# Optimization experiments

Measured on AMD Instinct MI355X. Metric: run time of the kernel, lower is better.

The kernel has to match this reference:

```python
import jax, jax.numpy as jnp
import numpy as np

STATE = 16
DT_RANK = 48
INNER = 1536
LN_EPS = 1e-5


def setup_inputs() -> dict:
    key = jax.random.key(0)
    ks = jax.random.split(key, 10)
    B, C, H, W = 128, 2048, 24, 12
    hid = 768
    inp = {}
    inp["x"] = jax.random.normal(ks[0], (B, C, H, W), jnp.float32)
    inp["pe_w"] = jax.random.normal(ks[1], (C, hid), jnp.float32) * 0.02
    inp["pe_b"] = jnp.zeros((hid,), jnp.float32)
    inp["ln_g"] = jnp.ones((hid,), jnp.float32)
    inp["ln_b"] = jnp.zeros((hid,), jnp.float32)
    inp["in_w"] = jax.random.normal(ks[2], (hid, 2 * INNER), jnp.float32) * 0.02
    inp["conv_w"] = jax.random.normal(ks[3], (INNER, 1, 3), jnp.float32) * 0.1
    inp["conv_b"] = jnp.zeros((INNER,), jnp.float32)
    # faithful init: A = repeat(arange(1, state+1)), A_log = log(A)
    inp["A_log"] = jnp.log(jnp.broadcast_to(jnp.arange(1, STATE + 1, dtype=jnp.float32), (INNER, STATE)))
    inp["xproj_w"] = jax.random.normal(ks[4], (INNER, DT_RANK + 2 * STATE), jnp.float32) * 0.02
    inp["dtproj_w"] = jax.random.normal(ks[5], (DT_RANK, INNER), jnp.float32) * 0.02
    inp["dtproj_b"] = jnp.zeros((INNER,), jnp.float32)
    inp["D_param"] = jnp.ones((INNER,), jnp.float32)
    inp["out_w"] = jax.random.normal(ks[6], (INNER, C), jnp.float32) * 0.02
    return inp


def _forward(x, pe_w, pe_b, ln_g, ln_b, in_w, conv_w, conv_b, A_log,
             xproj_w, dtproj_w, dtproj_b, D_param, out_w):
    B, C, H, W = x.shape
    # Patch_Embedding: AdaptiveAvgPool2d((3,3)) -- H,W divisible by 3 -> block mean
    xp = x.reshape(B, C, 3, H // 3, 3, W // 3).mean(axis=(3, 5))  # [B,C,3,3]
    tok = xp.reshape(B, C, 9).transpose(0, 2, 1)                   # [B,9,C]
    tok = tok @ pe_w + pe_b                                        # [B,9,hid]

    # Mamba: LayerNorm (biased variance)
    mu = tok.mean(-1, keepdims=True)
    var = tok.var(-1, keepdims=True)
    h = (tok - mu) / jnp.sqrt(var + LN_EPS) * ln_g + ln_b

    xz = h @ in_w                                                  # [B,9,2*inner]
    xs, z = xz[..., :INNER], xz[..., INNER:]

    # depthwise conv1d, kernel 3, pad 1
    xc = jax.lax.conv_general_dilated(
        xs.transpose(0, 2, 1), conv_w, window_strides=(1,), padding=[(1, 1)],
        feature_group_count=INNER, dimension_numbers=("NCH", "OIH", "NCH"))
    xc = (xc + conv_b[None, :, None]).transpose(0, 2, 1)           # [B,9,inner]
    xc = jax.nn.silu(xc)

    # SSM selective scan
    A = -jnp.exp(A_log)                                            # [inner,state]
    dbc = xc @ xproj_w                                             # [B,9,dtr+2*state]
    d_r = dbc[..., :DT_RANK]
    Bp = dbc[..., DT_RANK:DT_RANK + STATE]                         # [B,9,state]
    Cp = dbc[..., DT_RANK + STATE:]                                # [B,9,state]
    delta = jax.nn.softplus(d_r @ dtproj_w + dtproj_b)             # [B,9,inner]

    dA = jnp.exp(delta[..., None] * A)                             # [B,9,inner,state]
    dBu = delta[..., None] * Bp[:, :, None, :] * xc[..., None]     # [B,9,inner,state]

    def step(s, t):
        dA_i, dBu_i, C_i = t                                       # [B,inner,state],[B,inner,state],[B,state]
        s = dA_i * s + dBu_i
        y = jnp.einsum("bdn,bn->bd", s, C_i)
        return s, y

    s0 = jnp.zeros((B, INNER, STATE), xc.dtype)
    _, ys = jax.lax.scan(step, s0, (dA.transpose(1, 0, 2, 3),
                                    dBu.transpose(1, 0, 2, 3),
                                    Cp.transpose(1, 0, 2)))
    y = ys.transpose(1, 0, 2) + xc * D_param                       # [B,9,inner]

    y = y * jax.nn.silu(z)
    out = y @ out_w                                                # [B,9,C]

    # Inverse_Patch_Embedding: reshape to [B,C,3,3], bilinear upsample (align_corners=False)
    out = out.transpose(0, 2, 1).reshape(B, C, 3, 3)
    out = jax.image.resize(out, (B, C, H, W), method="bilinear")
    return out


def reference(x, pe_w, pe_b, ln_g, ln_b, in_w, conv_w, conv_b, A_log,
              xproj_w, dtproj_w, dtproj_b, D_param, out_w):
    return _forward(x, pe_w, pe_b, ln_g, ln_b, in_w, conv_w, conv_b, A_log,
                    xproj_w, dtproj_w, dtproj_b, D_param, out_w)
```

## Files before the change

kernel.cpp:

```cpp
#include <hip/hip_runtime.h>
#include <math.h>

#define Bn   128
#define Cn   2048
#define Hn   24
#define Wn   12
#define HID  768
#define NIN  1536
#define NST  16
#define DTR  48
#define Ln   9
#define Mn   (Bn*Ln)
#define XKS  16

typedef __bf16 bf16x8 __attribute__((ext_vector_type(8)));
typedef float  f32x4  __attribute__((ext_vector_type(4)));

#define GLOAD16(gsrc, ldst) \
  __builtin_amdgcn_global_load_lds((const __attribute__((address_space(1))) void*)(gsrc), \
                                   (__attribute__((address_space(3))) void*)(ldst), 16, 0, 0)

__device__ __forceinline__ unsigned short f2bf(float f) {
  unsigned u = __float_as_uint(f);
  u += 0x7fffu + ((u >> 16) & 1u);
  return (unsigned short)(u >> 16);
}
__device__ __forceinline__ float bf2f(unsigned short h) {
  return __uint_as_float(((unsigned)h) << 16);
}
__device__ __forceinline__ void split_bf(float f, unsigned short& hi, unsigned short& lo) {
  hi = f2bf(f);
  lo = f2bf(f - bf2f(hi));
}
__device__ __forceinline__ int col2(int k) { return ((k >> 5) << 6) + (k & 31); }

__global__ __launch_bounds__(256) void prep_kernel(const float* __restrict__ pe_w,
    const float* __restrict__ in_w, const float* __restrict__ out_w,
    const float* __restrict__ x,
    unsigned short* __restrict__ peT2, unsigned short* __restrict__ inT2,
    unsigned short* __restrict__ outT2, unsigned short* __restrict__ tok2) {
  __shared__ char smem[32 * 73 * 16];
  int bid = blockIdx.x;
  int t = threadIdx.x;
  if (bid < 6912) {
    float (*tile)[33] = reinterpret_cast<float (*)[33]>(smem);
    const float* W; unsigned short* T2; int K, N, nb, kb;
    if (bid < 1536)      { W = pe_w;  T2 = peT2;  K = Cn;  N = HID;     nb = bid % 24; kb = bid / 24; }
    else if (bid < 3840) { int q = bid - 1536; W = in_w;  T2 = inT2;  K = HID; N = 2 * NIN; nb = q % 96; kb = q / 96; }
    else                 { int q = bid - 3840; W = out_w; T2 = outT2; K = NIN; N = Cn;      nb = q % 64; kb = q / 64; }
    int kl = t >> 3, n4 = (t & 7) * 4;
    float4 v = *reinterpret_cast<const float4*>(W + (size_t)(kb * 32 + kl) * N + nb * 32 + n4);
    tile[kl][n4] = v.x; tile[kl][n4 + 1] = v.y; tile[kl][n4 + 2] = v.z; tile[kl][n4 + 3] = v.w;
    __syncthreads();
    int nl = t >> 3, k4 = (t & 7) * 4;
    unsigned short hi[4], lo[4];
    #pragma unroll
    for (int i = 0; i < 4; ++i) split_bf(tile[k4 + i][nl], hi[i], lo[i]);
    size_t base = (size_t)(nb * 32 + nl) * (2 * K) + kb * 64 + k4;
    uint2 ph, pl;
    ph.x = (unsigned)hi[0] | ((unsigned)hi[1] << 16);
    ph.y = (unsigned)hi[2] | ((unsigned)hi[3] << 16);
    pl.x = (unsigned)lo[0] | ((unsigned)lo[1] << 16);
    pl.y = (unsigned)lo[2] | ((unsigned)lo[3] << 16);
    *reinterpret_cast<uint2*>(T2 + base)      = ph;
    *reinterpret_cast<uint2*>(T2 + base + 32) = pl;
  } else {
    float4 (*raw)[73] = reinterpret_cast<float4 (*)[73]>(smem);
    int blk = bid - 6912;
    int b = blk >> 6, cg = blk & 63;
    const float4* src = reinterpret_cast<const float4*>(x) + (size_t)(b * Cn + cg * 32) * 72;
    #pragma unroll
    for (int it = 0; it < 9; ++it) {
      int li = it * 256 + t;
      raw[li / 72][li % 72] = src[li];
    }
    __syncthreads();
    for (int cell = t; cell < 288; cell += 256) {
      int c = cell / 9, p = cell % 9, i = p / 3, j = p % 3;
      float s = 0.f;
      #pragma unroll
      for (int k = 0; k < 8; ++k) {
        float4 v = raw[c][(i * 8 + k) * 3 + j];
        s += (v.x + v.y) + (v.z + v.w);
      }
      s *= (1.0f / 32.0f);
      unsigned short hi, lo;
      split_bf(s, hi, lo);
      int cglob = cg * 32 + c;
      size_t base = ((size_t)(b * Ln + p)) * (2 * Cn) + col2(cglob);
      tok2[base] = hi; tok2[base + 32] = lo;
    }
  }
}

__global__ __launch_bounds__(256) void mgemm_kernel(
    const unsigned short* __restrict__ A2, const unsigned short* __restrict__ B2,
    float* __restrict__ Cout, int M, int N, int K, int Ksub) {
  __shared__ unsigned short As[2][128][64];
  __shared__ unsigned short Bs[2][128][64];
  int t = threadIdx.x;
  int bm = blockIdx.y * 128, bn = blockIdx.x * 128;
  int wave = t >> 6, lane = t & 63;
  int wr = (wave >> 1) * 64, wc = (wave & 1) * 64;
  int lr = lane & 15, lk = lane >> 4;

  int l3 = lane >> 3, c8 = lane & 7;
  int sc = c8 ^ l3;
  size_t koff = (size_t)blockIdx.z * 2 * (size_t)Ksub;
  const unsigned short* Ab = A2 + (size_t)(bm + wave * 32 + l3) * (2 * (size_t)K) + koff + sc * 8;
  const unsigned short* Bb = B2 + (size_t)(bn + wave * 32 + l3) * (2 * (size_t)K) + koff + sc * 8;
  size_t rstep = (size_t)8 * 2 * K;

  f32x4 acc[4][4];
  #pragma unroll
  for (int m = 0; m < 4; ++m)
    #pragma unroll
    for (int n = 0; n < 4; ++n) acc[m][n] = {0.f, 0.f, 0.f, 0.f};

  {
    unsigned short* AsW = &As[0][wave * 32][0];
    unsigned short* BsW = &Bs[0][wave * 32][0];
    #pragma unroll
    for (int q = 0; q < 4; ++q) {
      GLOAD16(Ab + q * rstep, AsW + q * 8 * 64);
      GLOAD16(Bb + q * rstep, BsW + q * 8 * 64);
    }
  }
  __syncthreads();

  int cur = 0;
  for (int kk = 0; kk < Ksub; kk += 32) {
    if (kk + 32 < Ksub) {
      unsigned short* AsW = &As[cur ^ 1][wave * 32][0];
      unsigned short* BsW = &Bs[cur ^ 1][wave * 32][0];
      #pragma unroll
      for (int q = 0; q < 4; ++q) {
        GLOAD16(Ab + q * rstep + (kk + 32) * 2, AsW + q * 8 * 64);
        GLOAD16(Bb + q * rstep + (kk + 32) * 2, BsW + q * 8 * 64);
      }
    }

    bf16x8 ah[4], al[4], bh[4], bl[4];
    #pragma unroll
    for (int m = 0; m < 4; ++m) {
      int ar = wr + m * 16 + lr;
      ah[m] = *reinterpret_cast<const bf16x8*>(&As[cur][ar][((lk    ) ^ (ar & 7)) * 8]);
      al[m] = *reinterpret_cast<const bf16x8*>(&As[cur][ar][((4 + lk) ^ (ar & 7)) * 8]);
    }
    #pragma unroll
    for (int n = 0; n < 4; ++n) {
      int br = wc + n * 16 + lr;
      bh[n] = *reinterpret_cast<const bf16x8*>(&Bs[cur][br][((lk    ) ^ (br & 7)) * 8]);
      bl[n] = *reinterpret_cast<const bf16x8*>(&Bs[cur][br][((4 + lk) ^ (br & 7)) * 8]);
    }
    #pragma unroll
    for (int m = 0; m < 4; ++m)
      #pragma unroll
      for (int n = 0; n < 4; ++n) {
        acc[m][n] = __builtin_amdgcn_mfma_f32_16x16x32_bf16(ah[m], bh[n], acc[m][n], 0, 0, 0);
        acc[m][n] = __builtin_amdgcn_mfma_f32_16x16x32_bf16(ah[m], bl[n], acc[m][n], 0, 0, 0);
        acc[m][n] = __builtin_amdgcn_mfma_f32_16x16x32_bf16(al[m], bh[n], acc[m][n], 0, 0, 0);
      }
    __syncthreads();
    cur ^= 1;
  }

  float* dst = Cout + (size_t)blockIdx.z * M * N;
  #pragma unroll
  for (int m = 0; m < 4; ++m)
    #pragma unroll
    for (int n = 0; n < 4; ++n) {
      int col = bn + wc + n * 16 + lr;
      #pragma unroll
      for (int r = 0; r < 4; ++r) {
        int row = bm + wr + m * 16 + lk * 4 + r;
        dst[(size_t)row * N + col] = acc[m][n][r];
      }
    }
}

__device__ __forceinline__ float4 conv_silu4(const float* __restrict__ p0,
    const float* __restrict__ p1, const float* __restrict__ cw,
    const float* __restrict__ cb, int R, int d0) {
  int bq = R / 9, pq = R - bq * 9;
  size_t rb = (size_t)R * (2 * NIN) + d0;
  float4 a0 = *reinterpret_cast<const float4*>(p0 + rb);
  float4 a1 = *reinterpret_cast<const float4*>(p1 + rb);
  float cx[4] = {a0.x + a1.x, a0.y + a1.y, a0.z + a1.z, a0.w + a1.w};
  float cm[4] = {0.f, 0.f, 0.f, 0.f}, cp[4] = {0.f, 0.f, 0.f, 0.f};
  if (pq > 0) {
    float4 m0 = *reinterpret_cast<const float4*>(p0 + rb - 2 * NIN);
    float4 m1 = *reinterpret_cast<const float4*>(p1 + rb - 2 * NIN);
    cm[0] = m0.x + m1.x; cm[1] = m0.y + m1.y; cm[2] = m0.z + m1.z; cm[3] = m0.w + m1.w;
  }
  if (pq < Ln - 1) {
    float4 q0 = *reinterpret_cast<const float4*>(p0 + rb + 2 * NIN);
    float4 q1 = *reinterpret_cast<const float4*>(p1 + rb + 2 * NIN);
    cp[0] = q0.x + q1.x; cp[1] = q0.y + q1.y; cp[2] = q0.z + q1.z; cp[3] = q0.w + q1.w;
  }
  float4 w0 = *reinterpret_cast<const float4*>(cw + 3 * d0);
  float4 w1 = *reinterpret_cast<const float4*>(cw + 3 * d0 + 4);
  float4 w2 = *reinterpret_cast<const float4*>(cw + 3 * d0 + 8);
  float wf[12] = {w0.x, w0.y, w0.z, w0.w, w1.x, w1.y, w1.z, w1.w, w2.x, w2.y, w2.z, w2.w};
  float4 cb4 = *reinterpret_cast<const float4*>(cb + d0);
  float cbf[4] = {cb4.x, cb4.y, cb4.z, cb4.w};
  float r[4];
  #pragma unroll
  for (int i = 0; i < 4; ++i) {
    float a = cbf[i] + cm[i] * wf[3 * i] + cx[i] * wf[3 * i + 1] + cp[i] * wf[3 * i + 2];
    r[i] = a / (1.0f + __expf(-a));
  }
  return make_float4(r[0], r[1], r[2], r[3]);
}

__global__ __launch_bounds__(256) void xproj_kernel(const float* __restrict__ part2,
    const float* __restrict__ cw, const float* __restrict__ cb,
    const float* __restrict__ w, float* __restrict__ part) {
  __shared__ float at[64][44];
  __shared__ float wt[32][80];
  int kc = blockIdx.x, mt = blockIdx.y;
  int t = threadIdx.x;
  int tx = t & 15, ty = t >> 4;
  float acc[4][5] = {};
  int sr = t >> 3, sc4 = (t & 7) * 4;
  const float* p0 = part2;
  const float* p1 = part2 + (size_t)Mn * 2 * NIN;
  for (int k0 = kc * 96; k0 < kc * 96 + 96; k0 += 32) {
    float4 v0 = conv_silu4(p0, p1, cw, cb, mt * 64 + sr,      k0 + sc4);
    float4 v1 = conv_silu4(p0, p1, cw, cb, mt * 64 + sr + 32, k0 + sc4);
    __syncthreads();
    *reinterpret_cast<float4*>(&at[sr][sc4])      = v0;
    *reinterpret_cast<float4*>(&at[sr + 32][sc4]) = v1;
    for (int i = t; i < 32 * 80; i += 256)
      wt[i / 80][i % 80] = w[(size_t)(k0 + i / 80) * 80 + i % 80];
    __syncthreads();
    #pragma unroll
    for (int kk = 0; kk < 32; ++kk) {
      float a0[4], b0[5];
      #pragma unroll
      for (int i = 0; i < 4; ++i) a0[i] = at[ty * 4 + i][kk];
      #pragma unroll
      for (int j = 0; j < 5; ++j) b0[j] = wt[kk][tx + 16 * j];
      #pragma unroll
      for (int i = 0; i < 4; ++i)
        #pragma unroll
        for (int j = 0; j < 5; ++j)
          acc[i][j] = fmaf(a0[i], b0[j], acc[i][j]);
    }
  }
  #pragma unroll
  for (int i = 0; i < 4; ++i)
    #pragma unroll
    for (int j = 0; j < 5; ++j)
      part[((size_t)kc * Mn + mt * 64 + ty * 4 + i) * 80 + tx + 16 * j] = acc[i][j];
}

__global__ __launch_bounds__(256) void ln_kernel(const float* __restrict__ part1,
    const float* __restrict__ peb, const float* __restrict__ g, const float* __restrict__ be,
    unsigned short* __restrict__ h2) {
  int row = blockIdx.x;
  int t = threadIdx.x;
  float vq[3];
  #pragma unroll
  for (int q = 0; q < 3; ++q) {
    int c = t + q * 256;
    float v = peb[c];
    #pragma unroll
    for (int ks = 0; ks < 8; ++ks)
      v += part1[((size_t)ks * Mn + row) * HID + c];
    vq[q] = v;
  }
  float s  = vq[0] + vq[1] + vq[2];
  float s2 = vq[0] * vq[0] + vq[1] * vq[1] + vq[2] * vq[2];
  #pragma unroll
  for (int o = 32; o > 0; o >>= 1) {
    s  += __shfl_down(s,  o, 64);
    s2 += __shfl_down(s2, o, 64);
  }
  __shared__ float red[8];
  int wid = t >> 6, lane = t & 63;
  if (lane == 0) { red[wid] = s; red[4 + wid] = s2; }
  __syncthreads();
  float S  = red[0] + red[1] + red[2] + red[3];
  float S2 = red[4] + red[5] + red[6] + red[7];
  float mu  = S * (1.0f / HID);
  float var = S2 * (1.0f / HID) - mu * mu;
  float inv = rsqrtf(var + 1e-5f);
  #pragma unroll
  for (int q = 0; q < 3; ++q) {
    int c = t + q * 256;
    float hv = (vq[q] - mu) * inv * g[c] + be[c];
    unsigned short hi, lo;
    split_bf(hv, hi, lo);
    size_t base = (size_t)row * (2 * HID) + col2(c);
    h2[base] = hi; h2[base + 32] = lo;
  }
}

__global__ __launch_bounds__(256) void scan_kernel(const float* __restrict__ partx,
    const float* __restrict__ A_log, const float* __restrict__ Dp,
    const float* __restrict__ part2, const float* __restrict__ dtw,
    const float* __restrict__ dtb, const float* __restrict__ cw,
    const float* __restrict__ cb, unsigned short* __restrict__ ya2) {
  __shared__ float wdt[DTR * 256];
  __shared__ float dbc9[Ln][DTR];
  __shared__ float Bsh[Ln][NST], Csh[Ln][NST];
  int b      = blockIdx.x / (NIN / 256);
  int dchunk = blockIdx.x % (NIN / 256);
  int t = threadIdx.x;
  float4* w4 = reinterpret_cast<float4*>(wdt);
  #pragma unroll
  for (int it = 0; it < 12; ++it) {
    int i4 = it * 256 + t;
    int k = i4 >> 6, c4 = i4 & 63;
    w4[i4] = *reinterpret_cast<const float4*>(dtw + (size_t)k * NIN + dchunk * 256 + c4 * 4);
  }
  for (int i = t; i < Ln * 80; i += 256) {
    int p = i / 80, k = i - p * 80;
    size_t off = (size_t)(b * Ln + p) * 80 + k;
    float s = 0.f;
    #pragma unroll
    for (int ks = 0; ks < XKS; ++ks) s += partx[(size_t)ks * (Mn * 80) + off];
    if (k < DTR)            dbc9[p][k] = s;
    else if (k < DTR + NST) Bsh[p][k - DTR] = s;
    else                    Csh[p][k - DTR - NST] = s;
  }
  __syncthreads();
  int d = dchunk * 256 + t;
  float Ar[NST];
  #pragma unroll
  for (int n = 0; n < NST; ++n) Ar[n] = -__expf(A_log[(size_t)d * NST + n]);
  float s[NST];
  #pragma unroll
  for (int n = 0; n < NST; ++n) s[n] = 0.0f;
  float Dv = Dp[d];
  float bt = dtb[d];
  float w0 = cw[3 * d], w1 = cw[3 * d + 1], w2 = cw[3 * d + 2];
  float cbv = cb[d];
  int cc = col2(d);
  const float* px0 = part2 + d;
  const float* px1 = px0 + (size_t)Mn * 2 * NIN;
  const float* z0  = part2 + NIN + d;
  const float* z1  = z0 + (size_t)Mn * 2 * NIN;
  size_t row0 = (size_t)(b * Ln) * (2 * NIN);
  float xm = 0.f;
  float x0 = px0[row0] + px1[row0];
  for (int p = 0; p < Ln; ++p) {
    size_t roff = row0 + (size_t)p * (2 * NIN);
    float xp = 0.f;
    if (p < Ln - 1) xp = px0[roff + 2 * NIN] + px1[roff + 2 * NIN];
    float a0 = cbv + xm * w0 + x0 * w1 + xp * w2;
    float u = a0 / (1.0f + __expf(-a0));
    float a = bt;
    #pragma unroll
    for (int k = 0; k < DTR; ++k) a = fmaf(dbc9[p][k], wdt[k * 256 + t], a);
    float dl = fmaxf(a, 0.0f) + log1pf(__expf(-fabsf(a)));
    float du = dl * u;
    float y = 0.0f;
    #pragma unroll
    for (int n = 0; n < NST; ++n) {
      float dA = __expf(dl * Ar[n]);
      s[n] = dA * s[n] + du * Bsh[p][n];
      y += s[n] * Csh[p][n];
    }
    float zv = z0[roff] + z1[roff];
    float sz = zv / (1.0f + __expf(-zv));
    float yv = (y + u * Dv) * sz;
    unsigned short hi, lo;
    split_bf(yv, hi, lo);
    ya2[roff + cc] = hi; ya2[roff + cc + 32] = lo;
    xm = x0; x0 = xp;
  }
}

__global__ __launch_bounds__(256) void resize_kernel(const float* __restrict__ part3,
                                                     float* __restrict__ out) {
  __shared__ float v[32][10];
  int blk = blockIdx.x;
  int b = blk >> 6, cg = blk & 63;
  int t = threadIdx.x;
  size_t MN3 = (size_t)Mn * Cn;
  for (int i = t; i < 288; i += 256) {
    int p = i >> 5, c = i & 31;
    size_t base = (size_t)(b * Ln + p) * Cn + cg * 32 + c;
    v[c][p] = part3[base] + part3[base + MN3];
  }
  __syncthreads();
  int ch = t >> 3, sub = t & 7;
  float* dst = out + ((size_t)b * Cn + cg * 32 + ch) * 288;
  #pragma unroll
  for (int q = 0; q < 9; ++q) {
    int f = sub + q * 8;
    int y = f / 3, xq = f - y * 3;
    float fy  = (y + 0.5f) * 0.125f - 0.5f;
    float fyf = floorf(fy);
    float wy  = fy - fyf;
    int yy = (int)fyf;
    int y0 = min(2, max(0, yy)), y1 = min(2, max(0, yy + 1));
    float rr[3];
    #pragma unroll
    for (int j = 0; j < 3; ++j)
      rr[j] = v[ch][y0 * 3 + j] * (1.0f - wy) + v[ch][y1 * 3 + j] * wy;
    float ov[4];
    #pragma unroll
    for (int xi = 0; xi < 4; ++xi) {
      int xo = xq * 4 + xi;
      float fx  = (xo + 0.5f) * 0.25f - 0.5f;
      float fxf = floorf(fx);
      float wx  = fx - fxf;
      int xx = (int)fxf;
      int x0 = min(2, max(0, xx)), x1 = min(2, max(0, xx + 1));
      ov[xi] = rr[x0] * (1.0f - wx) + rr[x1] * wx;
    }
    *reinterpret_cast<float4*>(dst + f * 4) = make_float4(ov[0], ov[1], ov[2], ov[3]);
  }
}

extern "C" void kernel_launch(void* const* d_in, const int* in_sizes, int n_in,
                              void* d_out, int out_size, void* d_ws, size_t ws_size,
                              hipStream_t stream) {
  const float* x        = (const float*)d_in[0];
  const float* pe_w     = (const float*)d_in[1];
  const float* pe_b     = (const float*)d_in[2];
  const float* ln_g     = (const float*)d_in[3];
  const float* ln_b     = (const float*)d_in[4];
  const float* in_w     = (const float*)d_in[5];
  const float* conv_w   = (const float*)d_in[6];
  const float* conv_b   = (const float*)d_in[7];
  const float* A_log    = (const float*)d_in[8];
  const float* xproj_w  = (const float*)d_in[9];
  const float* dtproj_w = (const float*)d_in[10];
  const float* dtproj_b = (const float*)d_in[11];
  const float* D_param  = (const float*)d_in[12];
  const float* out_w    = (const float*)d_in[13];
  float* out = (float*)d_out;
  char* ws = (char*)d_ws;

  size_t o = 0;
  auto alloc = [&](size_t bytes) { size_t r = o; o += (bytes + 255) & ~(size_t)255; return r; };
  unsigned short* tok2  = (unsigned short*)(ws + alloc((size_t)Mn * 2 * Cn * 2));
  unsigned short* peT2  = (unsigned short*)(ws + alloc((size_t)HID * 2 * Cn * 2));
  unsigned short* inT2  = (unsigned short*)(ws + alloc((size_t)2 * NIN * 2 * HID * 2));
  unsigned short* outT2 = (unsigned short*)(ws + alloc((size_t)Cn * 2 * NIN * 2));
  unsigned short* h2    = (unsigned short*)(ws + alloc((size_t)Mn * 2 * HID * 2));
  unsigned short* ya2   = (unsigned short*)(ws + alloc((size_t)Mn * 2 * NIN * 2));
  float* part1 = (float*)(ws + alloc((size_t)8 * Mn * HID * 4));
  float* part2 = (float*)(ws + alloc((size_t)2 * Mn * 2 * NIN * 4));
  float* part3 = (float*)(ws + alloc((size_t)2 * Mn * Cn * 4));
  float* partx = (float*)(ws + alloc((size_t)XKS * Mn * 80 * 4));

  prep_kernel<<<15104, 256, 0, stream>>>(pe_w, in_w, out_w, x, peT2, inT2, outT2, tok2);

  mgemm_kernel<<<dim3(HID / 128, Mn / 128, 8), 256, 0, stream>>>(
      tok2, peT2, part1, Mn, HID, Cn, Cn / 8);
  ln_kernel<<<Mn, 256, 0, stream>>>(part1, pe_b, ln_g, ln_b, h2);
  mgemm_kernel<<<dim3(2 * NIN / 128, Mn / 128, 2), 256, 0, stream>>>(
      h2, inT2, part2, Mn, 2 * NIN, HID, HID / 2);
  xproj_kernel<<<dim3(XKS, Mn / 64), 256, 0, stream>>>(part2, conv_w, conv_b, xproj_w, partx);
  scan_kernel<<<Bn * (NIN / 256), 256, 0, stream>>>(
      partx, A_log, D_param, part2, dtproj_w, dtproj_b, conv_w, conv_b, ya2);
  mgemm_kernel<<<dim3(Cn / 128, Mn / 128, 2), 256, 0, stream>>>(
      ya2, outT2, part3, Mn, Cn, NIN, NIN / 2);
  resize_kernel<<<Bn * (Cn / 32), 256, 0, stream>>>(part3, out);
}
```

Baseline: 302.4 us.

## Halve GEMM M-tile to 64 and reduce or drop split-K partials

The MFMA GEMM block tile shrinks from 128x128 to 64x128, doubling the number of M blocks. Split-K drops from 8 to 4 for the patch-embed GEMM and is removed for the in-proj and out-proj GEMMs. Consumers now read a single output buffer instead of summing partials, which cuts fp32 partial write and read traffic. In exchange each block does less MFMA work per LDS load of B, and the in/out GEMMs run longer K loops per block with fewer blocks in the z dimension.

```diff
diff --git a/kernel.cpp b/kernel.cpp
--- a/kernel.cpp
+++ b/kernel.cpp
@@ -96,53 +96,51 @@
 __global__ __launch_bounds__(256) void mgemm_kernel(
     const unsigned short* __restrict__ A2, const unsigned short* __restrict__ B2,
     float* __restrict__ Cout, int M, int N, int K, int Ksub) {
-  __shared__ unsigned short As[2][128][64];
+  __shared__ unsigned short As[2][64][64];
   __shared__ unsigned short Bs[2][128][64];
   int t = threadIdx.x;
-  int bm = blockIdx.y * 128, bn = blockIdx.x * 128;
+  int bm = blockIdx.y * 64, bn = blockIdx.x * 128;
   int wave = t >> 6, lane = t & 63;
-  int wr = (wave >> 1) * 64, wc = (wave & 1) * 64;
+  int wr = (wave >> 1) * 32, wc = (wave & 1) * 64;
   int lr = lane & 15, lk = lane >> 4;
 
   int l3 = lane >> 3, c8 = lane & 7;
   int sc = c8 ^ l3;
   size_t koff = (size_t)blockIdx.z * 2 * (size_t)Ksub;
-  const unsigned short* Ab = A2 + (size_t)(bm + wave * 32 + l3) * (2 * (size_t)K) + koff + sc * 8;
+  const unsigned short* Ab = A2 + (size_t)(bm + wave * 16 + l3) * (2 * (size_t)K) + koff + sc * 8;
   const unsigned short* Bb = B2 + (size_t)(bn + wave * 32 + l3) * (2 * (size_t)K) + koff + sc * 8;
   size_t rstep = (size_t)8 * 2 * K;
 
-  f32x4 acc[4][4];
-  #pragma unroll
-  for (int m = 0; m < 4; ++m)
+  f32x4 acc[2][4];
+  #pragma unroll
+  for (int m = 0; m < 2; ++m)
     #pragma unroll
     for (int n = 0; n < 4; ++n) acc[m][n] = {0.f, 0.f, 0.f, 0.f};
 
   {
-    unsigned short* AsW = &As[0][wave * 32][0];
+    unsigned short* AsW = &As[0][wave * 16][0];
     unsigned short* BsW = &Bs[0][wave * 32][0];
     #pragma unroll
-    for (int q = 0; q < 4; ++q) {
-      GLOAD16(Ab + q * rstep, AsW + q * 8 * 64);
-      GLOAD16(Bb + q * rstep, BsW + q * 8 * 64);
-    }
+    for (int q = 0; q < 2; ++q) GLOAD16(Ab + q * rstep, AsW + q * 8 * 64);
+    #pragma unroll
+    for (int q = 0; q < 4; ++q) GLOAD16(Bb + q * rstep, BsW + q * 8 * 64);
   }
   __syncthreads();
 
   int cur = 0;
   for (int kk = 0; kk < Ksub; kk += 32) {
     if (kk + 32 < Ksub) {
-      unsigned short* AsW = &As[cur ^ 1][wave * 32][0];
+      unsigned short* AsW = &As[cur ^ 1][wave * 16][0];
       unsigned short* BsW = &Bs[cur ^ 1][wave * 32][0];
       #pragma unroll
-      for (int q = 0; q < 4; ++q) {
-        GLOAD16(Ab + q * rstep + (kk + 32) * 2, AsW + q * 8 * 64);
-        GLOAD16(Bb + q * rstep + (kk + 32) * 2, BsW + q * 8 * 64);
-      }
-    }
-
-    bf16x8 ah[4], al[4], bh[4], bl[4];
-    #pragma unroll
-    for (int m = 0; m < 4; ++m) {
+      for (int q = 0; q < 2; ++q) GLOAD16(Ab + q * rstep + (kk + 32) * 2, AsW + q * 8 * 64);
+      #pragma unroll
+      for (int q = 0; q < 4; ++q) GLOAD16(Bb + q * rstep + (kk + 32) * 2, BsW + q * 8 * 64);
+    }
+
+    bf16x8 ah[2], al[2], bh[4], bl[4];
+    #pragma unroll
+    for (int m = 0; m < 2; ++m) {
       int ar = wr + m * 16 + lr;
       ah[m] = *reinterpret_cast<const bf16x8*>(&As[cur][ar][((lk    ) ^ (ar & 7)) * 8]);
       al[m] = *reinterpret_cast<const bf16x8*>(&As[cur][ar][((4 + lk) ^ (ar & 7)) * 8]);
@@ -154,7 +152,7 @@
       bl[n] = *reinterpret_cast<const bf16x8*>(&Bs[cur][br][((4 + lk) ^ (br & 7)) * 8]);
     }
     #pragma unroll
-    for (int m = 0; m < 4; ++m)
+    for (int m = 0; m < 2; ++m)
       #pragma unroll
       for (int n = 0; n < 4; ++n) {
         acc[m][n] = __builtin_amdgcn_mfma_f32_16x16x32_bf16(ah[m], bh[n], acc[m][n], 0, 0, 0);
@@ -167,7 +165,7 @@
 
   float* dst = Cout + (size_t)blockIdx.z * M * N;
   #pragma unroll
-  for (int m = 0; m < 4; ++m)
+  for (int m = 0; m < 2; ++m)
     #pragma unroll
     for (int n = 0; n < 4; ++n) {
       int col = bn + wc + n * 16 + lr;
@@ -179,24 +177,20 @@
     }
 }
 
-__device__ __forceinline__ float4 conv_silu4(const float* __restrict__ p0,
-    const float* __restrict__ p1, const float* __restrict__ cw,
-    const float* __restrict__ cb, int R, int d0) {
+__device__ __forceinline__ float4 conv_silu4(const float* __restrict__ xz,
+    const float* __restrict__ cw, const float* __restrict__ cb, int R, int d0) {
   int bq = R / 9, pq = R - bq * 9;
   size_t rb = (size_t)R * (2 * NIN) + d0;
-  float4 a0 = *reinterpret_cast<const float4*>(p0 + rb);
-  float4 a1 = *reinterpret_cast<const float4*>(p1 + rb);
-  float cx[4] = {a0.x + a1.x, a0.y + a1.y, a0.z + a1.z, a0.w + a1.w};
+  float4 a0 = *reinterpret_cast<const float4*>(xz + rb);
+  float cx[4] = {a0.x, a0.y, a0.z, a0.w};
   float cm[4] = {0.f, 0.f, 0.f, 0.f}, cp[4] = {0.f, 0.f, 0.f, 0.f};
   if (pq > 0) {
-    float4 m0 = *reinterpret_cast<const float4*>(p0 + rb - 2 * NIN);
-    float4 m1 = *reinterpret_cast<const float4*>(p1 + rb - 2 * NIN);
-    cm[0] = m0.x + m1.x; cm[1] = m0.y + m1.y; cm[2] = m0.z + m1.z; cm[3] = m0.w + m1.w;
+    float4 m0 = *reinterpret_cast<const float4*>(xz + rb - 2 * NIN);
+    cm[0] = m0.x; cm[1] = m0.y; cm[2] = m0.z; cm[3] = m0.w;
   }
   if (pq < Ln - 1) {
-    float4 q0 = *reinterpret_cast<const float4*>(p0 + rb + 2 * NIN);
-    float4 q1 = *reinterpret_cast<const float4*>(p1 + rb + 2 * NIN);
-    cp[0] = q0.x + q1.x; cp[1] = q0.y + q1.y; cp[2] = q0.z + q1.z; cp[3] = q0.w + q1.w;
+    float4 q0 = *reinterpret_cast<const float4*>(xz + rb + 2 * NIN);
+    cp[0] = q0.x; cp[1] = q0.y; cp[2] = q0.z; cp[3] = q0.w;
   }
   float4 w0 = *reinterpret_cast<const float4*>(cw + 3 * d0);
   float4 w1 = *reinterpret_cast<const float4*>(cw + 3 * d0 + 4);
@@ -213,7 +207,7 @@
   return make_float4(r[0], r[1], r[2], r[3]);
 }
 
-__global__ __launch_bounds__(256) void xproj_kernel(const float* __restrict__ part2,
+__global__ __launch_bounds__(256) void xproj_kernel(const float* __restrict__ xz,
     const float* __restrict__ cw, const float* __restrict__ cb,
     const float* __restrict__ w, float* __restrict__ part) {
   __shared__ float at[64][44];
@@ -223,11 +217,9 @@
   int tx = t & 15, ty = t >> 4;
   float acc[4][5] = {};
   int sr = t >> 3, sc4 = (t & 7) * 4;
-  const float* p0 = part2;
-  const float* p1 = part2 + (size_t)Mn * 2 * NIN;
   for (int k0 = kc * 96; k0 < kc * 96 + 96; k0 += 32) {
-    float4 v0 = conv_silu4(p0, p1, cw, cb, mt * 64 + sr,      k0 + sc4);
-    float4 v1 = conv_silu4(p0, p1, cw, cb, mt * 64 + sr + 32, k0 + sc4);
+    float4 v0 = conv_silu4(xz, cw, cb, mt * 64 + sr,      k0 + sc4);
+    float4 v1 = conv_silu4(xz, cw, cb, mt * 64 + sr + 32, k0 + sc4);
     __syncthreads();
     *reinterpret_cast<float4*>(&at[sr][sc4])      = v0;
     *reinterpret_cast<float4*>(&at[sr + 32][sc4]) = v1;
@@ -266,7 +258,7 @@
     int c = t + q * 256;
     float v = peb[c];
     #pragma unroll
-    for (int ks = 0; ks < 8; ++ks)
+    for (int ks = 0; ks < 4; ++ks)
       v += part1[((size_t)ks * Mn + row) * HID + c];
     vq[q] = v;
   }
@@ -299,7 +291,7 @@
 
 __global__ __launch_bounds__(256) void scan_kernel(const float* __restrict__ partx,
     const float* __restrict__ A_log, const float* __restrict__ Dp,
-    const float* __restrict__ part2, const float* __restrict__ dtw,
+    const float* __restrict__ xz, const float* __restrict__ dtw,
     const float* __restrict__ dtb, const float* __restrict__ cw,
     const float* __restrict__ cb, unsigned short* __restrict__ ya2) {
   __shared__ float wdt[DTR * 256];
@@ -338,17 +330,15 @@
   float w0 = cw[3 * d], w1 = cw[3 * d + 1], w2 = cw[3 * d + 2];
   float cbv = cb[d];
   int cc = col2(d);
-  const float* px0 = part2 + d;
-  const float* px1 = px0 + (size_t)Mn * 2 * NIN;
-  const float* z0  = part2 + NIN + d;
-  const float* z1  = z0 + (size_t)Mn * 2 * NIN;
+  const float* px = xz + d;
+  const float* pz = xz + NIN + d;
   size_t row0 = (size_t)(b * Ln) * (2 * NIN);
   float xm = 0.f;
-  float x0 = px0[row0] + px1[row0];
+  float x0 = px[row0];
   for (int p = 0; p < Ln; ++p) {
     size_t roff = row0 + (size_t)p * (2 * NIN);
     float xp = 0.f;
-    if (p < Ln - 1) xp = px0[roff + 2 * NIN] + px1[roff + 2 * NIN];
+    if (p < Ln - 1) xp = px[roff + 2 * NIN];
     float a0 = cbv + xm * w0 + x0 * w1 + xp * w2;
     float u = a0 / (1.0f + __expf(-a0));
     float a = bt;
@@ -363,7 +353,7 @@
       s[n] = dA * s[n] + du * Bsh[p][n];
       y += s[n] * Csh[p][n];
     }
-    float zv = z0[roff] + z1[roff];
+    float zv = pz[roff];
     float sz = zv / (1.0f + __expf(-zv));
     float yv = (y + u * Dv) * sz;
     unsigned short hi, lo;
@@ -373,17 +363,15 @@
   }
 }
 
-__global__ __launch_bounds__(256) void resize_kernel(const float* __restrict__ part3,
+__global__ __launch_bounds__(256) void resize_kernel(const float* __restrict__ o9,
                                                      float* __restrict__ out) {
   __shared__ float v[32][10];
   int blk = blockIdx.x;
   int b = blk >> 6, cg = blk & 63;
   int t = threadIdx.x;
-  size_t MN3 = (size_t)Mn * Cn;
   for (int i = t; i < 288; i += 256) {
     int p = i >> 5, c = i & 31;
-    size_t base = (size_t)(b * Ln + p) * Cn + cg * 32 + c;
-    v[c][p] = part3[base] + part3[base + MN3];
+    v[c][p] = o9[(size_t)(b * Ln + p) * Cn + cg * 32 + c];
   }
   __syncthreads();
   int ch = t >> 3, sub = t & 7;
@@ -444,22 +432,22 @@
   unsigned short* outT2 = (unsigned short*)(ws + alloc((size_t)Cn * 2 * NIN * 2));
   unsigned short* h2    = (unsigned short*)(ws + alloc((size_t)Mn * 2 * HID * 2));
   unsigned short* ya2   = (unsigned short*)(ws + alloc((size_t)Mn * 2 * NIN * 2));
-  float* part1 = (float*)(ws + alloc((size_t)8 * Mn * HID * 4));
-  float* part2 = (float*)(ws + alloc((size_t)2 * Mn * 2 * NIN * 4));
-  float* part3 = (float*)(ws + alloc((size_t)2 * Mn * Cn * 4));
+  float* part1 = (float*)(ws + alloc((size_t)4 * Mn * HID * 4));
+  float* xz    = (float*)(ws + alloc((size_t)Mn * 2 * NIN * 4));
+  float* o9    = (float*)(ws + alloc((size_t)Mn * Cn * 4));
   float* partx = (float*)(ws + alloc((size_t)XKS * Mn * 80 * 4));
 
   prep_kernel<<<15104, 256, 0, stream>>>(pe_w, in_w, out_w, x, peT2, inT2, outT2, tok2);
 
-  mgemm_kernel<<<dim3(HID / 128, Mn / 128, 8), 256, 0, stream>>>(
-      tok2, peT2, part1, Mn, HID, Cn, Cn / 8);
+  mgemm_kernel<<<dim3(HID / 128, Mn / 64, 4), 256, 0, stream>>>(
+      tok2, peT2, part1, Mn, HID, Cn, Cn / 4);
   ln_kernel<<<Mn, 256, 0, stream>>>(part1, pe_b, ln_g, ln_b, h2);
-  mgemm_kernel<<<dim3(2 * NIN / 128, Mn / 128, 2), 256, 0, stream>>>(
-      h2, inT2, part2, Mn, 2 * NIN, HID, HID / 2);
-  xproj_kernel<<<dim3(XKS, Mn / 64), 256, 0, stream>>>(part2, conv_w, conv_b, xproj_w, partx);
+  mgemm_kernel<<<dim3(2 * NIN / 128, Mn / 64, 1), 256, 0, stream>>>(
+      h2, inT2, xz, Mn, 2 * NIN, HID, HID);
+  xproj_kernel<<<dim3(XKS, Mn / 64), 256, 0, stream>>>(xz, conv_w, conv_b, xproj_w, partx);
   scan_kernel<<<Bn * (NIN / 256), 256, 0, stream>>>(
-      partx, A_log, D_param, part2, dtproj_w, dtproj_b, conv_w, conv_b, ya2);
-  mgemm_kernel<<<dim3(Cn / 128, Mn / 128, 2), 256, 0, stream>>>(
-      ya2, outT2, part3, Mn, Cn, NIN, NIN / 2);
-  resize_kernel<<<Bn * (Cn / 32), 256, 0, stream>>>(part3, out);
-}
+      partx, A_log, D_param, xz, dtproj_w, dtproj_b, conv_w, conv_b, ya2);
+  mgemm_kernel<<<dim3(Cn / 128, Mn / 64, 1), 256, 0, stream>>>(
+      ya2, outT2, o9, Mn, Cn, NIN, NIN);
+  resize_kernel<<<Bn * (Cn / 32), 256, 0, stream>>>(o9, out);
+}
```

New measurement: 316.9 us. 4.8% more time.
